# Kernel tuning notes

Hardware: AMD Instinct MI355X
Metric: run time of the kernel (lower is better)

## Reference

```python
import jax, jax.numpy as jnp
import numpy as np

H = 7    # hidden dim
IN = 5   # input features
B = 8192
T = 512


def setup_inputs() -> dict:
    key = jax.random.key(0)
    ks = jax.random.split(key, 10)
    s = 1.0 / np.sqrt(H)  # torch default uniform bound for GRU/Linear
    u = lambda k, shape, b: jax.random.uniform(k, shape, jnp.float32, -b, b)
    return {
        "x": jax.random.normal(ks[0], (B, T, IN), dtype=jnp.float32),
        "batch_size": B,
        # GRU weights (torch layout: gates stacked [r; z; n] along dim 0)
        "W_ih": u(ks[1], (3 * H, IN), s),
        "W_hh": u(ks[2], (3 * H, H), s),
        "b_ih": u(ks[3], (3 * H,), s),
        "b_hh": u(ks[4], (3 * H,), s),
        # h0 = Linear(1, H, bias=False) applied to constant 1 -> weight column
        "W_h0": u(ks[5], (H, 1), 1.0),
        # output heads
        "W_m": u(ks[6], (3, H), s),
        "b_m": u(ks[7], (3,), s),
        "W_r": u(ks[8], (1, H), s),
        "b_r": u(ks[9], (1,), s),
    }


def reference(x, batch_size, W_ih, W_hh, b_ih, b_hh, W_h0, W_m, b_m, W_r, b_r):
    h_dim = W_hh.shape[1]
    # h_init = self.h0(ones(batch,1)) -> broadcast weight column  [B, H]
    h0 = jnp.broadcast_to(W_h0[:, 0], (batch_size, h_dim))
    # precompute input projection for all timesteps: [B, T, 3H]
    xp = jnp.einsum('bti,gi->btg', x, W_ih) + b_ih

    def step(h, xp_t):
        gh = h @ W_hh.T + b_hh                     # [B, 3H]
        xr, xz, xn = jnp.split(xp_t, 3, axis=-1)
        hr, hz, hn = jnp.split(gh, 3, axis=-1)
        r = jax.nn.sigmoid(xr + hr)
        z = jax.nn.sigmoid(xz + hz)
        n = jnp.tanh(xn + r * hn)
        h_new = (1.0 - z) * n + z * h
        return h_new, h_new

    h_last, all_h = jax.lax.scan(step, h0, jnp.swapaxes(xp, 0, 1))
    all_h = jnp.swapaxes(all_h, 0, 1)              # [B, T, H]
    # per-sample Linear heads in the original loop == one batched matmul
    out_m = all_h @ W_m.T + b_m                    # [B, T, 3]
    out_r = all_h @ W_r.T + b_r                    # [B, T, 1]
    return out_m, out_r, h_last[None]              # h_last: [1, B, H]
```

## Files before the change

kernel.cpp:

```cpp
#include <hip/hip_runtime.h>


namespace {
constexpr int Bn = 8192;
constexpr int Tn = 512;
constexpr int INn = 5;
constexpr int Hn = 7;
constexpr int TILE = 32;
constexpr int NTILE = Tn / TILE;
constexpr int BPB = 16;
constexpr int XSTR = 164;
constexpr long long OFF_OR = (long long)Bn * Tn * 3;
constexpr long long OFF_HL = OFF_OR + (long long)Bn * Tn;
constexpr float LOG2E = 1.44269504088896340736f;
}

typedef float v2f __attribute__((ext_vector_type(2)));

__device__ __forceinline__ v2f pk_fma(v2f a, v2f b, v2f c) {
    return __builtin_elementwise_fma(a, b, c);
}
__device__ __forceinline__ v2f splat2(float x) { return (v2f){x, x}; }

__device__ __forceinline__ float fast_sigmoid(float x) {
    float e = __builtin_amdgcn_exp2f(-LOG2E * x);
    return __builtin_amdgcn_rcpf(1.0f + e);
}
__device__ __forceinline__ float fast_tanh(float x) {
    float e = __builtin_amdgcn_exp2f(-2.0f * LOG2E * x);
    return __builtin_amdgcn_rcpf(1.0f + e) * 2.0f - 1.0f;
}

template<int CTRL>
__device__ __forceinline__ float dppf(float v) {
    int r = __builtin_amdgcn_update_dpp(0, __builtin_bit_cast(int, v),
                                        CTRL, 0xF, 0xF, true);
    return __builtin_bit_cast(float, r);
}

__global__ __launch_bounds__(256, 2) void gru_fused_kernel(
    const float* __restrict__ x,
    const float* __restrict__ W_ih,
    const float* __restrict__ W_hh,
    const float* __restrict__ b_ih,
    const float* __restrict__ b_hh,
    const float* __restrict__ W_h0,
    const float* __restrict__ W_m,
    const float* __restrict__ b_m,
    const float* __restrict__ W_r,
    const float* __restrict__ b_r,
    float* __restrict__ out)
{
    __shared__ float lds_x[2][BPB * XSTR];

    const int tid  = threadIdx.x;
    const int l    = tid & 15;
    const int j    = l & 7;
    const int g    = tid >> 4;
    const int b    = blockIdx.x * BPB + g;
    const int jj   = (j < 7) ? j : 6;
    const bool lo8 = ((l & 8) == 0);
    const bool hl  = (j == 7);

    const int row0 = lo8 ? jj : (Hn + jj);
    const int row1 = 2 * Hn + jj;

    v2f whh_rot[8];
    #pragma unroll
    for (int i = 0; i < 8; ++i) {
        const int k = (j - i) & 7;
        if (k < 7) {
            if (hl) {
                const float w0 = lo8 ? W_m[0 * Hn + k] : W_m[2 * Hn + k];
                const float w1 = lo8 ? W_m[1 * Hn + k] : W_r[k];
                whh_rot[i] = (v2f){w0, w1};
            } else {
                whh_rot[i] = (v2f){W_hh[row0 * Hn + k], W_hh[row1 * Hn + k]};
            }
        } else {
            whh_rot[i] = (v2f){0.0f, 0.0f};
        }
    }
    v2f wih01[INn];
    #pragma unroll
    for (int i = 0; i < INn; ++i)
        wih01[i] = hl ? (v2f){0.0f, 0.0f}
                      : (v2f){W_ih[row0 * INn + i], W_ih[row1 * INn + i]};
    const v2f biasH = hl ? (lo8 ? (v2f){b_m[0], b_m[1]}
                                : (v2f){b_m[2], b_r[0]})
                         : (v2f){b_hh[row0], b_hh[row1]};
    const v2f biasP = hl ? (v2f){0.0f, 0.0f}
                         : (v2f){b_ih[row0], b_ih[row1]};

    float hj = W_h0[jj];

    const float* xb = x + (long long)b * (Tn * INn);
    float* om  = out + (long long)b * (Tn * 3);
    float* orr = out + OFF_OR + (long long)b * Tn;

    float* hp0 = om - 3 + (lo8 ? 0 : 2);
    float* hp1 = lo8 ? (om - 2) : (orr - 1);
    const int hs1 = lo8 ? 3 : 1;

    float2 stage[5];
    #pragma unroll
    for (int i = 0; i < 5; ++i)
        stage[i] = *(const float2*)(xb + 2 * (l + 16 * i));

    int cur = 0;
    for (int tl = 0; tl < NTILE; ++tl) {
        #pragma unroll
        for (int i = 0; i < 5; ++i)
            *(float2*)&lds_x[cur][g * XSTR + 2 * (l + 16 * i)] = stage[i];
        __syncthreads();

        if (tl + 1 < NTILE) {
            const float* src = xb + (tl + 1) * (TILE * INn);
            #pragma unroll
            for (int i = 0; i < 5; ++i)
                stage[i] = *(const float2*)(src + 2 * (l + 16 * i));
        }

        const float4* xq = (const float4*)&lds_x[cur][g * XSTR];
        float4 xbuf[2][5];
        #pragma unroll
        for (int k = 0; k < 5; ++k) xbuf[0][k] = xq[k];

        #pragma unroll
        for (int c = 0; c < 8; ++c) {
            if (c < 7) {
                #pragma unroll
                for (int k = 0; k < 5; ++k)
                    xbuf[(c + 1) & 1][k] = xq[(c + 1) * 5 + k];
            }
            const float* xcf = (const float*)xbuf[c & 1];

            #pragma unroll
            for (int ss = 0; ss < 4; ++ss) {
                const int tt = c * 4 + ss;

                v2f accA = biasH;
                v2f accB = (v2f){0.0f, 0.0f};
                accA = pk_fma(whh_rot[0], splat2(hj), accA);
                {
                    float h1 = dppf<0x121>(hj);
                    accB = pk_fma(whh_rot[1], splat2(h1), accB);
                    float h2 = dppf<0x122>(hj);
                    accA = pk_fma(whh_rot[2], splat2(h2), accA);
                    float h3 = dppf<0x123>(hj);
                    accB = pk_fma(whh_rot[3], splat2(h3), accB);
                    float h4 = dppf<0x124>(hj);
                    accA = pk_fma(whh_rot[4], splat2(h4), accA);
                    float h5 = dppf<0x125>(hj);
                    accB = pk_fma(whh_rot[5], splat2(h5), accB);
                    float h6 = dppf<0x126>(hj);
                    accA = pk_fma(whh_rot[6], splat2(h6), accA);
                    float h7 = dppf<0x127>(hj);
                    accB = pk_fma(whh_rot[7], splat2(h7), accB);
                }
                v2f accH = accA + accB;

                v2f accP = biasP;
                #pragma unroll
                for (int i = 0; i < INn; ++i)
                    accP = pk_fma(wih01[i], splat2(xcf[5 * ss + i]), accP);

                if ((tl > 0 || tt > 0) && hl) {
                    *hp0 = accH[0];
                    *hp1 = accH[1];
                }
                hp0 += 3;
                hp1 += hs1;

                float s  = fast_sigmoid(accH[0] + accP[0]);
                float sv = dppf<0x128>(s);
                float r_val = lo8 ? s : sv;
                float z_val = lo8 ? sv : s;
                float n = fast_tanh(fmaf(r_val, accH[1], accP[1]));
                hj = n + z_val * (hj - n);
            }
        }
        cur ^= 1;
    }

    {
        v2f accA = biasH;
        v2f accB = (v2f){0.0f, 0.0f};
        accA = pk_fma(whh_rot[0], splat2(hj), accA);
        accB = pk_fma(whh_rot[1], splat2(dppf<0x121>(hj)), accB);
        accA = pk_fma(whh_rot[2], splat2(dppf<0x122>(hj)), accA);
        accB = pk_fma(whh_rot[3], splat2(dppf<0x123>(hj)), accB);
        accA = pk_fma(whh_rot[4], splat2(dppf<0x124>(hj)), accA);
        accB = pk_fma(whh_rot[5], splat2(dppf<0x125>(hj)), accB);
        accA = pk_fma(whh_rot[6], splat2(dppf<0x126>(hj)), accA);
        accB = pk_fma(whh_rot[7], splat2(dppf<0x127>(hj)), accB);
        v2f accH = accA + accB;
        if (hl) {
            *hp0 = accH[0];
            *hp1 = accH[1];
        }
    }

    if (l < Hn) out[OFF_HL + (long long)b * Hn + l] = hj;
}

extern "C" void kernel_launch(void* const* d_in, const int* in_sizes, int n_in,
                              void* d_out, int out_size, void* d_ws, size_t ws_size,
                              hipStream_t stream) {
    const float* x    = (const float*)d_in[0];
    const float* W_ih = (const float*)d_in[2];
    const float* W_hh = (const float*)d_in[3];
    const float* b_ih = (const float*)d_in[4];
    const float* b_hh = (const float*)d_in[5];
    const float* W_h0 = (const float*)d_in[6];
    const float* W_m  = (const float*)d_in[7];
    const float* b_m  = (const float*)d_in[8];
    const float* W_r  = (const float*)d_in[9];
    const float* b_r  = (const float*)d_in[10];
    float* out = (float*)d_out;

    dim3 grid(Bn / BPB);
    dim3 block(256);
    gru_fused_kernel<<<grid, block, 0, stream>>>(x, W_ih, W_hh, b_ih, b_hh,
                                                 W_h0, W_m, b_m, W_r, b_r, out);
}
```

Measured before the change: 234.1 us.

## Interleave two independent batch sequences per 16-lane group to hide latency

Each 16-lane group now advances two batch elements' GRU recurrences in lockstep, interleaving their DPP shuffles, packed FMAs and transcendentals so the two independent dependency chains can hide each other's latency. The block shrinks to 128 threads covering the same 16 sequences, and the launch bounds change to (128,1). This halves the number of wavefronts and roughly doubles per-thread register use, trading occupancy-based latency hiding for instruction-level parallelism.

```diff
diff --git a/kernel.cpp b/kernel.cpp
--- a/kernel.cpp
+++ b/kernel.cpp
@@ -22,10 +22,6 @@
 }
 __device__ __forceinline__ v2f splat2(float x) { return (v2f){x, x}; }
 
-__device__ __forceinline__ float fast_sigmoid(float x) {
-    float e = __builtin_amdgcn_exp2f(-LOG2E * x);
-    return __builtin_amdgcn_rcpf(1.0f + e);
-}
 __device__ __forceinline__ float fast_tanh(float x) {
     float e = __builtin_amdgcn_exp2f(-2.0f * LOG2E * x);
     return __builtin_amdgcn_rcpf(1.0f + e) * 2.0f - 1.0f;
@@ -38,7 +34,7 @@
     return __builtin_bit_cast(float, r);
 }
 
-__global__ __launch_bounds__(256, 2) void gru_fused_kernel(
+__global__ __launch_bounds__(128, 1) void gru_fused_kernel(
     const float* __restrict__ x,
     const float* __restrict__ W_ih,
     const float* __restrict__ W_hh,
@@ -57,7 +53,8 @@
     const int l    = tid & 15;
     const int j    = l & 7;
     const int g    = tid >> 4;
-    const int b    = blockIdx.x * BPB + g;
+    const int ba   = blockIdx.x * BPB + 2 * g;
+    const int bb   = ba + 1;
     const int jj   = (j < 7) ? j : 6;
     const bool lo8 = ((l & 8) == 0);
     const bool hl  = (j == 7);
@@ -92,116 +89,173 @@
     const v2f biasP = hl ? (v2f){0.0f, 0.0f}
                          : (v2f){b_ih[row0], b_ih[row1]};
 
-    float hj = W_h0[jj];
-
-    const float* xb = x + (long long)b * (Tn * INn);
-    float* om  = out + (long long)b * (Tn * 3);
-    float* orr = out + OFF_OR + (long long)b * Tn;
-
-    float* hp0 = om - 3 + (lo8 ? 0 : 2);
-    float* hp1 = lo8 ? (om - 2) : (orr - 1);
+    float ha = W_h0[jj];
+    float hb = ha;
+
+    const float* xap = x + (long long)ba * (Tn * INn);
+    const float* xbp = x + (long long)bb * (Tn * INn);
+
+    float* oma  = out + (long long)ba * (Tn * 3);
+    float* orra = out + OFF_OR + (long long)ba * Tn;
+    float* omb  = out + (long long)bb * (Tn * 3);
+    float* orrb = out + OFF_OR + (long long)bb * Tn;
+    float* hp0a = oma - 3 + (lo8 ? 0 : 2);
+    float* hp1a = lo8 ? (oma - 2) : (orra - 1);
+    float* hp0b = omb - 3 + (lo8 ? 0 : 2);
+    float* hp1b = lo8 ? (omb - 2) : (orrb - 1);
     const int hs1 = lo8 ? 3 : 1;
 
-    float2 stage[5];
+    float2 sta[5], stb[5];
     #pragma unroll
-    for (int i = 0; i < 5; ++i)
-        stage[i] = *(const float2*)(xb + 2 * (l + 16 * i));
+    for (int i = 0; i < 5; ++i) {
+        sta[i] = *(const float2*)(xap + 2 * (l + 16 * i));
+        stb[i] = *(const float2*)(xbp + 2 * (l + 16 * i));
+    }
 
     int cur = 0;
     for (int tl = 0; tl < NTILE; ++tl) {
         #pragma unroll
-        for (int i = 0; i < 5; ++i)
-            *(float2*)&lds_x[cur][g * XSTR + 2 * (l + 16 * i)] = stage[i];
+        for (int i = 0; i < 5; ++i) {
+            *(float2*)&lds_x[cur][(2 * g) * XSTR + 2 * (l + 16 * i)] = sta[i];
+            *(float2*)&lds_x[cur][(2 * g + 1) * XSTR + 2 * (l + 16 * i)] = stb[i];
+        }
         __syncthreads();
 
         if (tl + 1 < NTILE) {
-            const float* src = xb + (tl + 1) * (TILE * INn);
+            const float* srca = xap + (tl + 1) * (TILE * INn);
+            const float* srcb = xbp + (tl + 1) * (TILE * INn);
             #pragma unroll
-            for (int i = 0; i < 5; ++i)
-                stage[i] = *(const float2*)(src + 2 * (l + 16 * i));
-        }
-
-        const float4* xq = (const float4*)&lds_x[cur][g * XSTR];
-        float4 xbuf[2][5];
+            for (int i = 0; i < 5; ++i) {
+                sta[i] = *(const float2*)(srca + 2 * (l + 16 * i));
+                stb[i] = *(const float2*)(srcb + 2 * (l + 16 * i));
+            }
+        }
+
+        const float4* xqa = (const float4*)&lds_x[cur][(2 * g) * XSTR];
+        const float4* xqb = (const float4*)&lds_x[cur][(2 * g + 1) * XSTR];
+        float4 bufa[2][5], bufb[2][5];
         #pragma unroll
-        for (int k = 0; k < 5; ++k) xbuf[0][k] = xq[k];
+        for (int k = 0; k < 5; ++k) { bufa[0][k] = xqa[k]; bufb[0][k] = xqb[k]; }
 
         #pragma unroll
         for (int c = 0; c < 8; ++c) {
             if (c < 7) {
                 #pragma unroll
-                for (int k = 0; k < 5; ++k)
-                    xbuf[(c + 1) & 1][k] = xq[(c + 1) * 5 + k];
-            }
-            const float* xcf = (const float*)xbuf[c & 1];
+                for (int k = 0; k < 5; ++k) {
+                    bufa[(c + 1) & 1][k] = xqa[(c + 1) * 5 + k];
+                    bufb[(c + 1) & 1][k] = xqb[(c + 1) * 5 + k];
+                }
+            }
+            const float* xaf = (const float*)bufa[c & 1];
+            const float* xbf = (const float*)bufb[c & 1];
 
             #pragma unroll
             for (int ss = 0; ss < 4; ++ss) {
                 const int tt = c * 4 + ss;
 
-                v2f accA = biasH;
-                v2f accB = (v2f){0.0f, 0.0f};
-                accA = pk_fma(whh_rot[0], splat2(hj), accA);
+                v2f aA = biasH, aB = (v2f){0.0f, 0.0f};
+                v2f bA = biasH, bB = (v2f){0.0f, 0.0f};
+                aA = pk_fma(whh_rot[0], splat2(ha), aA);
+                bA = pk_fma(whh_rot[0], splat2(hb), bA);
                 {
-                    float h1 = dppf<0x121>(hj);
-                    accB = pk_fma(whh_rot[1], splat2(h1), accB);
-                    float h2 = dppf<0x122>(hj);
-                    accA = pk_fma(whh_rot[2], splat2(h2), accA);
-                    float h3 = dppf<0x123>(hj);
-                    accB = pk_fma(whh_rot[3], splat2(h3), accB);
-                    float h4 = dppf<0x124>(hj);
-                    accA = pk_fma(whh_rot[4], splat2(h4), accA);
-                    float h5 = dppf<0x125>(hj);
-                    accB = pk_fma(whh_rot[5], splat2(h5), accB);
-                    float h6 = dppf<0x126>(hj);
-                    accA = pk_fma(whh_rot[6], splat2(h6), accA);
-                    float h7 = dppf<0x127>(hj);
-                    accB = pk_fma(whh_rot[7], splat2(h7), accB);
-                }
-                v2f accH = accA + accB;
-
-                v2f accP = biasP;
+                    float t0 = dppf<0x121>(ha);
+                    float u0 = dppf<0x121>(hb);
+                    aB = pk_fma(whh_rot[1], splat2(t0), aB);
+                    bB = pk_fma(whh_rot[1], splat2(u0), bB);
+                    float t1 = dppf<0x122>(ha);
+                    float u1 = dppf<0x122>(hb);
+                    aA = pk_fma(whh_rot[2], splat2(t1), aA);
+                    bA = pk_fma(whh_rot[2], splat2(u1), bA);
+                    float t2 = dppf<0x123>(ha);
+                    float u2 = dppf<0x123>(hb);
+                    aB = pk_fma(whh_rot[3], splat2(t2), aB);
+                    bB = pk_fma(whh_rot[3], splat2(u2), bB);
+                    float t3 = dppf<0x124>(ha);
+                    float u3 = dppf<0x124>(hb);
+                    aA = pk_fma(whh_rot[4], splat2(t3), aA);
+                    bA = pk_fma(whh_rot[4], splat2(u3), bA);
+                    float t4 = dppf<0x125>(ha);
+                    float u4 = dppf<0x125>(hb);
+                    aB = pk_fma(whh_rot[5], splat2(t4), aB);
+                    bB = pk_fma(whh_rot[5], splat2(u4), bB);
+                    float t5 = dppf<0x126>(ha);
+                    float u5 = dppf<0x126>(hb);
+                    aA = pk_fma(whh_rot[6], splat2(t5), aA);
+                    bA = pk_fma(whh_rot[6], splat2(u5), bA);
+                    float t6 = dppf<0x127>(ha);
+                    float u6 = dppf<0x127>(hb);
+                    aB = pk_fma(whh_rot[7], splat2(t6), aB);
+                    bB = pk_fma(whh_rot[7], splat2(u6), bB);
+                }
+                v2f accHa = aA + aB;
+                v2f accHb = bA + bB;
+
+                v2f accPa = biasP, accPb = biasP;
                 #pragma unroll
-                for (int i = 0; i < INn; ++i)
-                    accP = pk_fma(wih01[i], splat2(xcf[5 * ss + i]), accP);
+                for (int i = 0; i < INn; ++i) {
+                    accPa = pk_fma(wih01[i], splat2(xaf[5 * ss + i]), accPa);
+                    accPb = pk_fma(wih01[i], splat2(xbf[5 * ss + i]), accPb);
+                }
 
                 if ((tl > 0 || tt > 0) && hl) {
-                    *hp0 = accH[0];
-                    *hp1 = accH[1];
-                }
-                hp0 += 3;
-                hp1 += hs1;
-
-                float s  = fast_sigmoid(accH[0] + accP[0]);
-                float sv = dppf<0x128>(s);
-                float r_val = lo8 ? s : sv;
-                float z_val = lo8 ? sv : s;
-                float n = fast_tanh(fmaf(r_val, accH[1], accP[1]));
-                hj = n + z_val * (hj - n);
+                    *hp0a = accHa[0];
+                    *hp1a = accHa[1];
+                    *hp0b = accHb[0];
+                    *hp1b = accHb[1];
+                }
+                hp0a += 3; hp1a += hs1;
+                hp0b += 3; hp1b += hs1;
+
+                float ea = __builtin_amdgcn_exp2f(-LOG2E * (accHa[0] + accPa[0]));
+                float eb = __builtin_amdgcn_exp2f(-LOG2E * (accHb[0] + accPb[0]));
+                float sa = __builtin_amdgcn_rcpf(1.0f + ea);
+                float sb = __builtin_amdgcn_rcpf(1.0f + eb);
+                float sva = dppf<0x128>(sa);
+                float svb = dppf<0x128>(sb);
+                float rva = lo8 ? sa : sva;
+                float rvb = lo8 ? sb : svb;
+                float zva = lo8 ? sva : sa;
+                float zvb = lo8 ? svb : sb;
+                float na = fast_tanh(fmaf(rva, accHa[1], accPa[1]));
+                float nb = fast_tanh(fmaf(rvb, accHb[1], accPb[1]));
+                ha = na + zva * (ha - na);
+                hb = nb + zvb * (hb - nb);
             }
         }
         cur ^= 1;
     }
 
     {
-        v2f accA = biasH;
-        v2f accB = (v2f){0.0f, 0.0f};
-        accA = pk_fma(whh_rot[0], splat2(hj), accA);
-        accB = pk_fma(whh_rot[1], splat2(dppf<0x121>(hj)), accB);
-        accA = pk_fma(whh_rot[2], splat2(dppf<0x122>(hj)), accA);
-        accB = pk_fma(whh_rot[3], splat2(dppf<0x123>(hj)), accB);
-        accA = pk_fma(whh_rot[4], splat2(dppf<0x124>(hj)), accA);
-        accB = pk_fma(whh_rot[5], splat2(dppf<0x125>(hj)), accB);
-        accA = pk_fma(whh_rot[6], splat2(dppf<0x126>(hj)), accA);
-        accB = pk_fma(whh_rot[7], splat2(dppf<0x127>(hj)), accB);
-        v2f accH = accA + accB;
+        v2f aA = biasH, aB = (v2f){0.0f, 0.0f};
+        v2f bA = biasH, bB = (v2f){0.0f, 0.0f};
+        aA = pk_fma(whh_rot[0], splat2(ha), aA);
+        bA = pk_fma(whh_rot[0], splat2(hb), bA);
+        aB = pk_fma(whh_rot[1], splat2(dppf<0x121>(ha)), aB);
+        bB = pk_fma(whh_rot[1], splat2(dppf<0x121>(hb)), bB);
+        aA = pk_fma(whh_rot[2], splat2(dppf<0x122>(ha)), aA);
+        bA = pk_fma(whh_rot[2], splat2(dppf<0x122>(hb)), bA);
+        aB = pk_fma(whh_rot[3], splat2(dppf<0x123>(ha)), aB);
+        bB = pk_fma(whh_rot[3], splat2(dppf<0x123>(hb)), bB);
+        aA = pk_fma(whh_rot[4], splat2(dppf<0x124>(ha)), aA);
+        bA = pk_fma(whh_rot[4], splat2(dppf<0x124>(hb)), bA);
+        aB = pk_fma(whh_rot[5], splat2(dppf<0x125>(ha)), aB);
+        bB = pk_fma(whh_rot[5], splat2(dppf<0x125>(hb)), bB);
+        aA = pk_fma(whh_rot[6], splat2(dppf<0x126>(ha)), aA);
+        bA = pk_fma(whh_rot[6], splat2(dppf<0x126>(hb)), bA);
+        aB = pk_fma(whh_rot[7], splat2(dppf<0x127>(ha)), aB);
+        bB = pk_fma(whh_rot[7], splat2(dppf<0x127>(hb)), bB);
+        v2f accHa = aA + aB;
+        v2f accHb = bA + bB;
         if (hl) {
-            *hp0 = accH[0];
-            *hp1 = accH[1];
-        }
-    }
-
-    if (l < Hn) out[OFF_HL + (long long)b * Hn + l] = hj;
+            *hp0a = accHa[0];
+            *hp1a = accHa[1];
+            *hp0b = accHb[0];
+            *hp1b = accHb[1];
+        }
+    }
+
+    if (l < Hn) out[OFF_HL + (long long)ba * Hn + l] = ha;
+    if (l >= 8 && l < 8 + Hn) out[OFF_HL + (long long)bb * Hn + (l - 8)] = hb;
 }
 
 extern "C" void kernel_launch(void* const* d_in, const int* in_sizes, int n_in,
@@ -220,7 +274,7 @@
     float* out = (float*)d_out;
 
     dim3 grid(Bn / BPB);
-    dim3 block(256);
+    dim3 block(128);
     gru_fused_kernel<<<grid, block, 0, stream>>>(x, W_ih, W_hh, b_ih, b_hh,
                                                  W_h0, W_m, b_m, W_r, b_r, out);
 }
```

New measurement: 249.4 us. 6.5% more time.

## Stream x directly from global into registers and fold exp scaling into weights

Applied to the files above, without the earlier changes.

Removes the LDS double buffer and __syncthreads by having each 16-lane group load its x timesteps straight from global memory into a 4-deep float4 register ring, prefetched three chunks ahead. The -log2e and -2log2e factors for sigmoid and tanh are folded into the hidden and input weights and biases at setup, removing a multiply per activation on the serial recurrence path. Output pointers are now computed by index per tile instead of incremented each step. The cost is more registers and redundant global loads of the same x data by all 16 lanes of a group, which may pressure occupancy or cache bandwidth.

```diff
diff --git a/kernel.cpp b/kernel.cpp
--- a/kernel.cpp
+++ b/kernel.cpp
@@ -6,10 +6,9 @@
 constexpr int Tn = 512;
 constexpr int INn = 5;
 constexpr int Hn = 7;
-constexpr int TILE = 32;
-constexpr int NTILE = Tn / TILE;
 constexpr int BPB = 16;
-constexpr int XSTR = 164;
+constexpr int NTILE = 16;
+constexpr int CPT = 8;
 constexpr long long OFF_OR = (long long)Bn * Tn * 3;
 constexpr long long OFF_HL = OFF_OR + (long long)Bn * Tn;
 constexpr float LOG2E = 1.44269504088896340736f;
@@ -21,15 +20,6 @@
     return __builtin_elementwise_fma(a, b, c);
 }
 __device__ __forceinline__ v2f splat2(float x) { return (v2f){x, x}; }
-
-__device__ __forceinline__ float fast_sigmoid(float x) {
-    float e = __builtin_amdgcn_exp2f(-LOG2E * x);
-    return __builtin_amdgcn_rcpf(1.0f + e);
-}
-__device__ __forceinline__ float fast_tanh(float x) {
-    float e = __builtin_amdgcn_exp2f(-2.0f * LOG2E * x);
-    return __builtin_amdgcn_rcpf(1.0f + e) * 2.0f - 1.0f;
-}
 
 template<int CTRL>
 __device__ __forceinline__ float dppf(float v) {
@@ -51,8 +41,6 @@
     const float* __restrict__ b_r,
     float* __restrict__ out)
 {
-    __shared__ float lds_x[2][BPB * XSTR];
-
     const int tid  = threadIdx.x;
     const int l    = tid & 15;
     const int j    = l & 7;
@@ -61,6 +49,11 @@
     const int jj   = (j < 7) ? j : 6;
     const bool lo8 = ((l & 8) == 0);
     const bool hl  = (j == 7);
+    const bool is7  = hl && lo8;
+    const bool is15 = hl && !lo8;
+
+    const float kR = -LOG2E;
+    const float kN = -2.0f * LOG2E;
 
     const int row0 = lo8 ? jj : (Hn + jj);
     const int row1 = 2 * Hn + jj;
@@ -75,7 +68,8 @@
                 const float w1 = lo8 ? W_m[1 * Hn + k] : W_r[k];
                 whh_rot[i] = (v2f){w0, w1};
             } else {
-                whh_rot[i] = (v2f){W_hh[row0 * Hn + k], W_hh[row1 * Hn + k]};
+                whh_rot[i] = (v2f){kR * W_hh[row0 * Hn + k],
+                                   kN * W_hh[row1 * Hn + k]};
             }
         } else {
             whh_rot[i] = (v2f){0.0f, 0.0f};
@@ -85,55 +79,42 @@
     #pragma unroll
     for (int i = 0; i < INn; ++i)
         wih01[i] = hl ? (v2f){0.0f, 0.0f}
-                      : (v2f){W_ih[row0 * INn + i], W_ih[row1 * INn + i]};
+                      : (v2f){kR * W_ih[row0 * INn + i],
+                              kN * W_ih[row1 * INn + i]};
     const v2f biasH = hl ? (lo8 ? (v2f){b_m[0], b_m[1]}
                                 : (v2f){b_m[2], b_r[0]})
-                         : (v2f){b_hh[row0], b_hh[row1]};
+                         : (v2f){kR * b_hh[row0], kN * b_hh[row1]};
     const v2f biasP = hl ? (v2f){0.0f, 0.0f}
-                         : (v2f){b_ih[row0], b_ih[row1]};
+                         : (v2f){kR * b_ih[row0], kN * b_ih[row1]};
 
     float hj = W_h0[jj];
 
-    const float* xb = x + (long long)b * (Tn * INn);
+    const float4* xq = (const float4*)(x + (long long)b * (Tn * INn));
     float* om  = out + (long long)b * (Tn * 3);
     float* orr = out + OFF_OR + (long long)b * Tn;
 
-    float* hp0 = om - 3 + (lo8 ? 0 : 2);
-    float* hp1 = lo8 ? (om - 2) : (orr - 1);
-    const int hs1 = lo8 ? 3 : 1;
-
-    float2 stage[5];
+    float4 xbuf[4][5];
     #pragma unroll
-    for (int i = 0; i < 5; ++i)
-        stage[i] = *(const float2*)(xb + 2 * (l + 16 * i));
-
-    int cur = 0;
+    for (int k = 0; k < 5; ++k) {
+        xbuf[0][k] = xq[k];
+        xbuf[1][k] = xq[5 + k];
+        xbuf[2][k] = xq[10 + k];
+    }
+
     for (int tl = 0; tl < NTILE; ++tl) {
+        float* mb0 = om + (tl * 96 - 3) + (lo8 ? 0 : 2);
+        float* mb1 = om + (tl * 96 - 3) + 1;
+        float* rb  = orr + (tl * 32 - 1);
+        const float4* xpre = xq + tl * (CPT * 5) + 15;
+
         #pragma unroll
-        for (int i = 0; i < 5; ++i)
-            *(float2*)&lds_x[cur][g * XSTR + 2 * (l + 16 * i)] = stage[i];
-        __syncthreads();
-
-        if (tl + 1 < NTILE) {
-            const float* src = xb + (tl + 1) * (TILE * INn);
-            #pragma unroll
-            for (int i = 0; i < 5; ++i)
-                stage[i] = *(const float2*)(src + 2 * (l + 16 * i));
-        }
-
-        const float4* xq = (const float4*)&lds_x[cur][g * XSTR];
-        float4 xbuf[2][5];
-        #pragma unroll
-        for (int k = 0; k < 5; ++k) xbuf[0][k] = xq[k];
-
-        #pragma unroll
-        for (int c = 0; c < 8; ++c) {
-            if (c < 7) {
+        for (int c = 0; c < CPT; ++c) {
+            if (c <= 4 || tl + 1 < NTILE) {
                 #pragma unroll
                 for (int k = 0; k < 5; ++k)
-                    xbuf[(c + 1) & 1][k] = xq[(c + 1) * 5 + k];
+                    xbuf[(c + 3) & 3][k] = xpre[c * 5 + k];
             }
-            const float* xcf = (const float*)xbuf[c & 1];
+            const float* xcf = (const float*)xbuf[c & 3];
 
             #pragma unroll
             for (int ss = 0; ss < 4; ++ss) {
@@ -165,22 +146,23 @@
                 for (int i = 0; i < INn; ++i)
                     accP = pk_fma(wih01[i], splat2(xcf[5 * ss + i]), accP);
 
-                if ((tl > 0 || tt > 0) && hl) {
-                    *hp0 = accH[0];
-                    *hp1 = accH[1];
+                if (tt > 0 || tl > 0) {
+                    if (hl)   mb0[3 * tt] = accH[0];
+                    if (is7)  mb1[3 * tt] = accH[1];
+                    if (is15) rb[tt]      = accH[1];
                 }
-                hp0 += 3;
-                hp1 += hs1;
-
-                float s  = fast_sigmoid(accH[0] + accP[0]);
+
+                float ea = __builtin_amdgcn_exp2f(accH[0] + accP[0]);
+                float s  = __builtin_amdgcn_rcpf(1.0f + ea);
                 float sv = dppf<0x128>(s);
-                float r_val = lo8 ? s : sv;
-                float z_val = lo8 ? sv : s;
-                float n = fast_tanh(fmaf(r_val, accH[1], accP[1]));
-                hj = n + z_val * (hj - n);
+                float rv = lo8 ? s : sv;
+                float zv = lo8 ? sv : s;
+                float et = __builtin_amdgcn_exp2f(fmaf(rv, accH[1], accP[1]));
+                float t  = __builtin_amdgcn_rcpf(1.0f + et);
+                float n  = fmaf(2.0f, t, -1.0f);
+                hj = n + zv * (hj - n);
             }
         }
-        cur ^= 1;
     }
 
     {
@@ -195,10 +177,9 @@
         accA = pk_fma(whh_rot[6], splat2(dppf<0x126>(hj)), accA);
         accB = pk_fma(whh_rot[7], splat2(dppf<0x127>(hj)), accB);
         v2f accH = accA + accB;
-        if (hl) {
-            *hp0 = accH[0];
-            *hp1 = accH[1];
-        }
+        if (hl)   om[(Tn - 1) * 3 + (lo8 ? 0 : 2)] = accH[0];
+        if (is7)  om[(Tn - 1) * 3 + 1]             = accH[1];
+        if (is15) orr[Tn - 1]                      = accH[1];
     }
 
     if (l < Hn) out[OFF_HL + (long long)b * Hn + l] = hj;
```

Result: slower. 274.5 us (+17.3%).

## Stage head outputs in LDS and write coalesced per tile; fold exp scales into weights

Applied to the files above, without the earlier changes.

Head outputs were previously written with scattered per-timestep stores from two lanes per group. They now go into a per-group LDS buffer and are flushed once per 32-step tile as coalesced stores across all 16 lanes. The -log2e and -2log2e factors are also pre-multiplied into the GRU weights and biases, which removes multiplies from the serial recurrence. The LDS flush has no explicit barrier between writes and reads within the group, and it adds LDS traffic plus some index arithmetic.

```diff
diff --git a/kernel.cpp b/kernel.cpp
--- a/kernel.cpp
+++ b/kernel.cpp
@@ -10,6 +10,7 @@
 constexpr int NTILE = Tn / TILE;
 constexpr int BPB = 16;
 constexpr int XSTR = 164;
+constexpr int HSTR = 132;
 constexpr long long OFF_OR = (long long)Bn * Tn * 3;
 constexpr long long OFF_HL = OFF_OR + (long long)Bn * Tn;
 constexpr float LOG2E = 1.44269504088896340736f;
@@ -21,15 +22,6 @@
     return __builtin_elementwise_fma(a, b, c);
 }
 __device__ __forceinline__ v2f splat2(float x) { return (v2f){x, x}; }
-
-__device__ __forceinline__ float fast_sigmoid(float x) {
-    float e = __builtin_amdgcn_exp2f(-LOG2E * x);
-    return __builtin_amdgcn_rcpf(1.0f + e);
-}
-__device__ __forceinline__ float fast_tanh(float x) {
-    float e = __builtin_amdgcn_exp2f(-2.0f * LOG2E * x);
-    return __builtin_amdgcn_rcpf(1.0f + e) * 2.0f - 1.0f;
-}
 
 template<int CTRL>
 __device__ __forceinline__ float dppf(float v) {
@@ -52,6 +44,7 @@
     float* __restrict__ out)
 {
     __shared__ float lds_x[2][BPB * XSTR];
+    __shared__ float lds_h[BPB * HSTR];
 
     const int tid  = threadIdx.x;
     const int l    = tid & 15;
@@ -61,6 +54,10 @@
     const int jj   = (j < 7) ? j : 6;
     const bool lo8 = ((l & 8) == 0);
     const bool hl  = (j == 7);
+    const bool is15 = hl && !lo8;
+
+    const float kR = -LOG2E;
+    const float kN = -2.0f * LOG2E;
 
     const int row0 = lo8 ? jj : (Hn + jj);
     const int row1 = 2 * Hn + jj;
@@ -75,7 +72,8 @@
                 const float w1 = lo8 ? W_m[1 * Hn + k] : W_r[k];
                 whh_rot[i] = (v2f){w0, w1};
             } else {
-                whh_rot[i] = (v2f){W_hh[row0 * Hn + k], W_hh[row1 * Hn + k]};
+                whh_rot[i] = (v2f){kR * W_hh[row0 * Hn + k],
+                                   kN * W_hh[row1 * Hn + k]};
             }
         } else {
             whh_rot[i] = (v2f){0.0f, 0.0f};
@@ -85,12 +83,13 @@
     #pragma unroll
     for (int i = 0; i < INn; ++i)
         wih01[i] = hl ? (v2f){0.0f, 0.0f}
-                      : (v2f){W_ih[row0 * INn + i], W_ih[row1 * INn + i]};
+                      : (v2f){kR * W_ih[row0 * INn + i],
+                              kN * W_ih[row1 * INn + i]};
     const v2f biasH = hl ? (lo8 ? (v2f){b_m[0], b_m[1]}
                                 : (v2f){b_m[2], b_r[0]})
-                         : (v2f){b_hh[row0], b_hh[row1]};
+                         : (v2f){kR * b_hh[row0], kN * b_hh[row1]};
     const v2f biasP = hl ? (v2f){0.0f, 0.0f}
-                         : (v2f){b_ih[row0], b_ih[row1]};
+                         : (v2f){kR * b_ih[row0], kN * b_ih[row1]};
 
     float hj = W_h0[jj];
 
@@ -98,9 +97,14 @@
     float* om  = out + (long long)b * (Tn * 3);
     float* orr = out + OFF_OR + (long long)b * Tn;
 
-    float* hp0 = om - 3 + (lo8 ? 0 : 2);
-    float* hp1 = lo8 ? (om - 2) : (orr - 1);
-    const int hs1 = lo8 ? 3 : 1;
+    float* hwb = &lds_h[g * HSTR + (is15 ? 66 : 0)];
+    const float* hrd = &lds_h[g * HSTR];
+    int fq[6];
+    #pragma unroll
+    for (int i = 0; i < 6; ++i) {
+        const int q = i * 16 + l;
+        fq[i] = (q % 3) * 33 + q / 3;
+    }
 
     float2 stage[5];
     #pragma unroll
@@ -165,20 +169,35 @@
                 for (int i = 0; i < INn; ++i)
                     accP = pk_fma(wih01[i], splat2(xcf[5 * ss + i]), accP);
 
-                if ((tl > 0 || tt > 0) && hl) {
-                    *hp0 = accH[0];
-                    *hp1 = accH[1];
+                if (hl) {
+                    hwb[tt]      = accH[0];
+                    hwb[33 + tt] = accH[1];
                 }
-                hp0 += 3;
-                hp1 += hs1;
-
-                float s  = fast_sigmoid(accH[0] + accP[0]);
+
+                float ea = __builtin_amdgcn_exp2f(accH[0] + accP[0]);
+                float s  = __builtin_amdgcn_rcpf(1.0f + ea);
                 float sv = dppf<0x128>(s);
-                float r_val = lo8 ? s : sv;
-                float z_val = lo8 ? sv : s;
-                float n = fast_tanh(fmaf(r_val, accH[1], accP[1]));
-                hj = n + z_val * (hj - n);
-            }
+                float rv = lo8 ? s : sv;
+                float zv = lo8 ? sv : s;
+                float et = __builtin_amdgcn_exp2f(fmaf(rv, accH[1], accP[1]));
+                float t  = __builtin_amdgcn_rcpf(1.0f + et);
+                float n  = fmaf(2.0f, t, -1.0f);
+                hj = n + zv * (hj - n);
+            }
+        }
+
+        {
+            float* omt = om + tl * 96 - 3;
+            float* ort = orr + tl * 32 - 1;
+            #pragma unroll
+            for (int i = 0; i < 6; ++i) {
+                float v = hrd[fq[i]];
+                if (tl > 0 || i > 0 || l >= 3) omt[i * 16 + l] = v;
+            }
+            float v0 = hrd[99 + l];
+            float v1 = hrd[99 + 16 + l];
+            if (tl > 0 || l > 0) ort[l] = v0;
+            ort[16 + l] = v1;
         }
         cur ^= 1;
     }
@@ -195,10 +214,9 @@
         accA = pk_fma(whh_rot[6], splat2(dppf<0x126>(hj)), accA);
         accB = pk_fma(whh_rot[7], splat2(dppf<0x127>(hj)), accB);
         v2f accH = accA + accB;
-        if (hl) {
-            *hp0 = accH[0];
-            *hp1 = accH[1];
-        }
+        if (hl)  om[(Tn - 1) * 3 + (lo8 ? 0 : 2)] = accH[0];
+        if (hl && lo8) om[(Tn - 1) * 3 + 1] = accH[1];
+        if (is15)      orr[Tn - 1]          = accH[1];
     }
 
     if (l < Hn) out[OFF_HL + (long long)b * Hn + l] = hj;
```

After: 219.9 us. -6.1%, faster.
